# Kernel tuning notes

Measured on AMD Instinct MI355X. Metric: run time of the kernel, lower is better.

Reference implementation:

```python
import jax, jax.numpy as jnp
import numpy as np

BN_EPS = 1e-5


def _bn_relu(x, gamma, beta):
    # training-mode BatchNorm1d over (batch, length) per channel; x: [B,C,N]
    mean = jnp.mean(x, axis=(0, 2), keepdims=True)
    var = jnp.var(x, axis=(0, 2), keepdims=True)  # biased, matching torch normalization
    xh = (x - mean) * jax.lax.rsqrt(var + BN_EPS)
    return jax.nn.relu(xh * gamma[None, :, None] + beta[None, :, None])


def setup_inputs() -> dict:
    key = jax.random.key(0)
    ks = jax.random.split(key, 12)
    B, N, S, C1, C2 = 16, 4096, 1024, 256, 256
    C_in = C1 + C2  # 512
    M0, M1 = 256, 256  # mlp channels
    return {
        "xyz1": jax.random.normal(ks[0], (B, 3, N), dtype=jnp.float32),
        "xyz2": jax.random.normal(ks[1], (B, 3, S), dtype=jnp.float32),
        "points1": jax.random.normal(ks[2], (B, C1, N), dtype=jnp.float32),
        "points2": jax.random.normal(ks[3], (B, C2, S), dtype=jnp.float32),
        "w0": jax.random.normal(ks[4], (M0, C_in), dtype=jnp.float32) * 0.02,
        "b0": jnp.zeros((M0,), dtype=jnp.float32),
        "g0": jnp.ones((M0,), dtype=jnp.float32),
        "be0": jnp.zeros((M0,), dtype=jnp.float32),
        "w1": jax.random.normal(ks[5], (M1, M0), dtype=jnp.float32) * 0.02,
        "b1": jnp.zeros((M1,), dtype=jnp.float32),
        "g1": jnp.ones((M1,), dtype=jnp.float32),
        "be1": jnp.zeros((M1,), dtype=jnp.float32),
    }


def reference(xyz1, xyz2, points1, points2, w0, b0, g0, be0, w1, b1, g1, be1):
    # xyz1: [B,3,N], xyz2: [B,3,S], points1: [B,C1,N], points2: [B,C2,S]
    xyz1_t = xyz1.transpose(0, 2, 1)  # [B,N,3]
    xyz2_t = xyz2.transpose(0, 2, 1)  # [B,S,3]
    p2_t = points2.transpose(0, 2, 1)  # [B,S,C2]

    # squared pairwise distances [B,N,S] via |a|^2 + |b|^2 - 2ab
    d = (jnp.sum(xyz1_t ** 2, -1)[:, :, None]
         + jnp.sum(xyz2_t ** 2, -1)[:, None, :]
         - 2.0 * jnp.einsum('bnd,bsd->bns', xyz1_t, xyz2_t))

    # 3 nearest neighbours (smallest distances)
    neg_d3, idx = jax.lax.top_k(-d, 3)  # [B,N,3]
    dists = -neg_d3

    recip = 1.0 / (dists + 1e-8)
    weight = recip / jnp.sum(recip, axis=-1, keepdims=True)  # [B,N,3]

    gathered = jax.vmap(lambda p, i: p[i])(p2_t, idx)  # [B,N,3,C2]
    interp = jnp.sum(gathered * weight[..., None], axis=2)  # [B,N,C2]

    new_points = jnp.concatenate([points1.transpose(0, 2, 1), interp], axis=-1)  # [B,N,C1+C2]
    x = new_points.transpose(0, 2, 1)  # [B,C_in,N]

    # 1x1 Conv1d == per-position matmul
    x = _bn_relu(jnp.einsum('oi,bin->bon', w0, x) + b0[None, :, None], g0, be0)
    x = _bn_relu(jnp.einsum('oi,bin->bon', w1, x) + b1[None, :, None], g1, be1)
    return x
```

## Files before the change

### kernel.cpp

```cpp
#include <hip/hip_runtime.h>
#include <stdint.h>

using u16 = unsigned short;
using short8 = __attribute__((ext_vector_type(8))) short;
using f32x4  = __attribute__((ext_vector_type(4))) float;
using u32x4  = __attribute__((ext_vector_type(4))) unsigned int;

__device__ __forceinline__ float bf2f(u16 u) {
  return __builtin_bit_cast(float, ((unsigned)u) << 16);
}
__device__ __forceinline__ u16 f2bf(float f) {
  unsigned u = __builtin_bit_cast(unsigned, f);
  u += 0x7FFFu + ((u >> 16) & 1u);
  return (u16)(u >> 16);
}

__device__ __forceinline__ void ins3(float& d0, float& d1, float& d2,
                                     int& i0, int& i1, int& i2, float d, int s) {
  bool c0 = d < d0, c1 = d < d1, c2 = d < d2;
  d2 = c1 ? d1 : (c2 ? d : d2);
  i2 = c1 ? i1 : (c2 ? s : i2);
  d1 = c0 ? d0 : (c1 ? d : d1);
  i1 = c0 ? i0 : (c1 ? s : i1);
  d0 = c0 ? d : d0;
  i0 = c0 ? s : i0;
}

__global__ __launch_bounds__(256, 8) void nn3_kernel(
    const float* __restrict__ xyz1, const float* __restrict__ xyz2,
    int* __restrict__ idx_out, float* __restrict__ w_out) {
  __shared__ __align__(16) float cand[8 * 516];
  const int b = blockIdx.y;
  const int t = threadIdx.x;
  const float* x2 = xyz2 + b * 3072;
  for (int i = t; i < 1024; i += 256) {
    float x = x2[i], y = x2[1024 + i], z = x2[2048 + i];
    f32x4 v = { -2.0f * x, -2.0f * y, -2.0f * z, x*x + y*y + z*z };
    *(f32x4*)&cand[(i >> 7) * 516 + (i & 127) * 4] = v;
  }
  __syncthreads();
  const int q = t >> 3, sub = t & 7;
  const int n = blockIdx.x * 32 + q;
  const float* x1 = xyz1 + b * 12288;
  const float px = x1[n], py = x1[4096 + n], pz = x1[8192 + n];
  float d0 = 1e30f, d1 = 1e30f, d2 = 1e30f;
  int i0 = 0, i1 = 0, i2 = 0;
  const int sbeg = sub << 7;
  const float* reg = &cand[sub * 516];
  #pragma unroll 4
  for (int ii = 0; ii < 128; ++ii) {
    f32x4 c = *(const f32x4*)(reg + ii * 4);
    float d = __builtin_fmaf(px, c[0],
              __builtin_fmaf(py, c[1],
              __builtin_fmaf(pz, c[2], c[3])));
    ins3(d0, d1, d2, i0, i1, i2, d, sbeg + ii);
  }
  for (int st = 1; st <= 4; st <<= 1) {
    float e0 = __shfl_xor(d0, st), e1 = __shfl_xor(d1, st), e2 = __shfl_xor(d2, st);
    int   j0 = __shfl_xor(i0, st), j1 = __shfl_xor(i1, st), j2 = __shfl_xor(i2, st);
    ins3(d0, d1, d2, i0, i1, i2, e0, j0);
    ins3(d0, d1, d2, i0, i1, i2, e1, j1);
    ins3(d0, d1, d2, i0, i1, i2, e2, j2);
  }
  if (sub == 0) {
    const float r1 = px*px + py*py + pz*pz;
    float w0 = 1.0f/(d0 + r1 + 1e-8f), w1 = 1.0f/(d1 + r1 + 1e-8f), w2 = 1.0f/(d2 + r1 + 1e-8f);
    float inv = 1.0f/(w0 + w1 + w2);
    const int pos = b * 4096 + n;
    idx_out[pos*3+0] = i0; idx_out[pos*3+1] = i1; idx_out[pos*3+2] = i2;
    w_out[pos*3+0] = w0*inv; w_out[pos*3+1] = w1*inv; w_out[pos*3+2] = w2*inv;
  }
}

__global__ __launch_bounds__(256) void transpose_cl(
    const float* __restrict__ in, u16* __restrict__ out, int L, int rstride) {
  __shared__ u16 tile[64][66];
  const int b = blockIdx.z;
  in  += (size_t)b * 256 * L;
  out += (size_t)b * L * rstride;
  const int n0 = blockIdx.x * 64, c0 = blockIdx.y * 64;
  const int t = threadIdx.x, ln = t & 63, grp = t >> 6;
  for (int p = 0; p < 16; ++p) {
    int cc = p*4 + grp;
    tile[cc][ln] = f2bf(in[(size_t)(c0 + cc) * L + n0 + ln]);
  }
  __syncthreads();
  for (int p = 0; p < 16; ++p) {
    int nn = p*4 + grp;
    out[(size_t)(n0 + nn) * rstride + c0 + ln] = tile[ln][nn];
  }
}

__global__ __launch_bounds__(256) void cvt_kernel(const float* __restrict__ in,
                                                  u16* __restrict__ out, int n) {
  int i = blockIdx.x * 256 + threadIdx.x;
  if (i < n) out[i] = f2bf(in[i]);
}

__global__ __launch_bounds__(256) void interp_kernel(
    const u16* __restrict__ p2t, const int* __restrict__ idx,
    const float* __restrict__ wgt, u16* __restrict__ A1) {
  const int t = threadIdx.x;
  const int base = blockIdx.x * 16;
  for (int i = 0; i < 16; ++i) {
    const int pos = base + i;
    const int b = pos >> 12;
    const int j0 = idx[pos*3+0], j1 = idx[pos*3+1], j2 = idx[pos*3+2];
    const float w0 = wgt[pos*3+0], w1 = wgt[pos*3+1], w2 = wgt[pos*3+2];
    const u16* r0 = p2t + ((size_t)(b*1024 + j0)) * 256;
    const u16* r1 = p2t + ((size_t)(b*1024 + j1)) * 256;
    const u16* r2 = p2t + ((size_t)(b*1024 + j2)) * 256;
    float v = w0*bf2f(r0[t]) + w1*bf2f(r1[t]) + w2*bf2f(r2[t]);
    A1[(size_t)pos*512 + 256 + t] = f2bf(v);
  }
}

__global__ __launch_bounds__(256) void gemm_kernel(
    const u16* __restrict__ A, const u16* __restrict__ Bw,
    const float* __restrict__ bias, u16* __restrict__ Y, int K) {
  __shared__ __align__(16) u16 As[128*48];
  __shared__ __align__(16) u16 Bs[128*48];
  const int t = threadIdx.x;
  const int m0 = blockIdx.x * 128, n0 = blockIdx.y * 128;
  const int wave = t >> 6, l = t & 63;
  const int wm = wave & 1, wn = wave >> 1;
  const int lc = l & 15, quad = l >> 4;
  f32x4 acc[4][4] = {};
  const int rowA = t >> 2, kc = (t & 3) * 8;
  for (int k0 = 0; k0 < K; k0 += 32) {
    *(u32x4*)&As[rowA*48 + kc]      = *(const u32x4*)&A[(size_t)(m0 + rowA)*K + k0 + kc];
    *(u32x4*)&As[(rowA+64)*48 + kc] = *(const u32x4*)&A[(size_t)(m0 + rowA + 64)*K + k0 + kc];
    *(u32x4*)&Bs[rowA*48 + kc]      = *(const u32x4*)&Bw[(size_t)(n0 + rowA)*K + k0 + kc];
    *(u32x4*)&Bs[(rowA+64)*48 + kc] = *(const u32x4*)&Bw[(size_t)(n0 + rowA + 64)*K + k0 + kc];
    __syncthreads();
    short8 af[4], bfv[4];
    for (int tm = 0; tm < 4; ++tm)
      af[tm] = *(const short8*)&As[(wm*64 + tm*16 + lc)*48 + quad*8];
    for (int tn = 0; tn < 4; ++tn)
      bfv[tn] = *(const short8*)&Bs[(wn*64 + tn*16 + lc)*48 + quad*8];
    for (int tm = 0; tm < 4; ++tm)
      for (int tn = 0; tn < 4; ++tn)
        acc[tm][tn] = __builtin_amdgcn_mfma_f32_16x16x32_bf16(af[tm], bfv[tn], acc[tm][tn], 0, 0, 0);
    __syncthreads();
  }
  for (int tn = 0; tn < 4; ++tn) {
    const int col = n0 + wn*64 + tn*16 + lc;
    const float bb = bias[col];
    for (int tm = 0; tm < 4; ++tm) {
      const int row = m0 + wm*64 + tm*16 + quad*4;
      for (int r = 0; r < 4; ++r)
        Y[(size_t)(row + r)*256 + col] = f2bf(acc[tm][tn][r] + bb);
    }
  }
}

__global__ __launch_bounds__(256) void colstats_kernel(
    const u16* __restrict__ Y, float* __restrict__ sums, float* __restrict__ sumsq) {
  const int t = threadIdx.x;
  size_t base = (size_t)blockIdx.x * 256 * 256;
  float s = 0.0f, q = 0.0f;
  for (int r = 0; r < 256; ++r) {
    float v = bf2f(Y[base + (size_t)r*256 + t]);
    s += v; q += v*v;
  }
  atomicAdd(&sums[t], s);
  atomicAdd(&sumsq[t], q);
}

__global__ void bnprep_kernel(const float* __restrict__ sums, const float* __restrict__ sumsq,
                              const float* __restrict__ g, const float* __restrict__ be,
                              float* __restrict__ scale, float* __restrict__ shift) {
  const int t = threadIdx.x;
  const float inv_n = 1.0f / 65536.0f;
  float mean = sums[t] * inv_n;
  float var = sumsq[t] * inv_n - mean*mean;
  float a = g[t] * rsqrtf(var + 1e-5f);
  scale[t] = a;
  shift[t] = be[t] - mean * a;
}

__global__ __launch_bounds__(256) void bnrelu_kernel(
    const u16* __restrict__ Y, const float* __restrict__ scale,
    const float* __restrict__ shift, u16* __restrict__ X) {
  const int t = threadIdx.x;
  const float a = scale[t], s = shift[t];
  size_t base = (size_t)blockIdx.x * 16 * 256;
  for (int r = 0; r < 16; ++r) {
    float v = bf2f(Y[base + r*256 + t]) * a + s;
    X[base + r*256 + t] = f2bf(v > 0.0f ? v : 0.0f);
  }
}

__global__ __launch_bounds__(256) void bnrelu_tr_kernel(
    const u16* __restrict__ Y, const float* __restrict__ scale,
    const float* __restrict__ shift, float* __restrict__ out) {
  __shared__ u16 tile[256][66];
  const int t = threadIdx.x;
  const int b = blockIdx.z;
  const int n0 = blockIdx.x * 64;
  const float a = scale[t], s = shift[t];
  for (int nn = 0; nn < 64; ++nn) {
    size_t pos = (size_t)b*4096 + n0 + nn;
    float v = bf2f(Y[pos*256 + t]) * a + s;
    tile[t][nn] = f2bf(v > 0.0f ? v : 0.0f);
  }
  __syncthreads();
  const int ln = t & 63, grp = t >> 6;
  for (int p = 0; p < 64; ++p) {
    int oo = p*4 + grp;
    out[((size_t)b*256 + oo)*4096 + n0 + ln] = bf2f(tile[oo][ln]);
  }
}

extern "C" void kernel_launch(void* const* d_in, const int* in_sizes, int n_in,
                              void* d_out, int out_size, void* d_ws, size_t ws_size,
                              hipStream_t stream) {
  const float* xyz1    = (const float*)d_in[0];
  const float* xyz2    = (const float*)d_in[1];
  const float* points1 = (const float*)d_in[2];
  const float* points2 = (const float*)d_in[3];
  const float* w0      = (const float*)d_in[4];
  const float* b0      = (const float*)d_in[5];
  const float* g0      = (const float*)d_in[6];
  const float* be0     = (const float*)d_in[7];
  const float* w1      = (const float*)d_in[8];
  const float* b1      = (const float*)d_in[9];
  const float* g1      = (const float*)d_in[10];
  const float* be1     = (const float*)d_in[11];
  float* out = (float*)d_out;

  char* ws = (char*)d_ws;
  u16*   A1   = (u16*)ws;
  u16*   X0   = (u16*)ws;
  u16*   Y    = (u16*)(ws + (64ull  << 20));
  u16*   p2t  = (u16*)(ws + (96ull  << 20));
  int*   idxb = (int*)(ws + (104ull << 20));
  float* wgtb = (float*)(ws + (105ull << 20));
  u16*   w0b  = (u16*)(ws + (106ull << 20));
  u16*   w1b  = (u16*)(ws + (106ull << 20) + (256u << 10));
  float* stats= (float*)(ws + (106ull << 20) + (512u << 10));

  float* sums0 = stats, *sumsq0 = stats + 256, *scale0 = stats + 512, *shift0 = stats + 768;
  float* sums1 = stats + 1024, *sumsq1 = stats + 1280, *scale1 = stats + 1536, *shift1 = stats + 1792;

  hipMemsetAsync(stats, 0, 2048 * sizeof(float), stream);
  nn3_kernel<<<dim3(128, 16), 256, 0, stream>>>(xyz1, xyz2, idxb, wgtb);
  transpose_cl<<<dim3(16, 4, 16), 256, 0, stream>>>(points2, p2t, 1024, 256);
  transpose_cl<<<dim3(64, 4, 16), 256, 0, stream>>>(points1, A1, 4096, 512);
  cvt_kernel<<<512, 256, 0, stream>>>(w0, w0b, 131072);
  cvt_kernel<<<256, 256, 0, stream>>>(w1, w1b, 65536);
  interp_kernel<<<4096, 256, 0, stream>>>(p2t, idxb, wgtb, A1);
  gemm_kernel<<<dim3(512, 2), 256, 0, stream>>>(A1, w0b, b0, Y, 512);
  colstats_kernel<<<256, 256, 0, stream>>>(Y, sums0, sumsq0);
  bnprep_kernel<<<1, 256, 0, stream>>>(sums0, sumsq0, g0, be0, scale0, shift0);
  bnrelu_kernel<<<4096, 256, 0, stream>>>(Y, scale0, shift0, X0);
  gemm_kernel<<<dim3(512, 2), 256, 0, stream>>>(X0, w1b, b1, Y, 256);
  colstats_kernel<<<256, 256, 0, stream>>>(Y, sums1, sumsq1);
  bnprep_kernel<<<1, 256, 0, stream>>>(sums1, sumsq1, g1, be1, scale1, shift1);
  bnrelu_tr_kernel<<<dim3(64, 1, 16), 256, 0, stream>>>(Y, scale1, shift1, out);
}
```

Baseline: 324.5 us.

## Fuse BN column stats into GEMM epilogue, use direct-to-LDS loads, vectorize BN-ReLU

The GEMM now loads tiles with global_load_lds straight into unpadded LDS, and its epilogue accumulates per-column sum and sum-of-squares, reduced with shuffles and atomics. This removes both separate colstats passes over Y. The bnrelu kernel now processes four channels per thread with 64-bit loads and stores. The cost is more atomics per GEMM block, possible LDS bank conflicts from dropping the padding, and stats computed from fp32 values rather than the rounded bf16 output.

```diff
diff --git a/kernel.cpp b/kernel.cpp
--- a/kernel.cpp
+++ b/kernel.cpp
@@ -5,6 +5,13 @@
 using short8 = __attribute__((ext_vector_type(8))) short;
 using f32x4  = __attribute__((ext_vector_type(4))) float;
 using u32x4  = __attribute__((ext_vector_type(4))) unsigned int;
+
+typedef const __attribute__((address_space(1))) unsigned int gas_u32;
+typedef __attribute__((address_space(3))) unsigned int las_u32;
+
+__device__ __forceinline__ void gload16(const void* g, void* l) {
+  __builtin_amdgcn_global_load_lds((gas_u32*)g, (las_u32*)l, 16, 0, 0);
+}
 
 __device__ __forceinline__ float bf2f(u16 u) {
   return __builtin_bit_cast(float, ((unsigned)u) << 16);
@@ -117,27 +124,33 @@
 
 __global__ __launch_bounds__(256) void gemm_kernel(
     const u16* __restrict__ A, const u16* __restrict__ Bw,
-    const float* __restrict__ bias, u16* __restrict__ Y, int K) {
-  __shared__ __align__(16) u16 As[128*48];
-  __shared__ __align__(16) u16 Bs[128*48];
+    const float* __restrict__ bias, u16* __restrict__ Y, int K,
+    float* __restrict__ sums, float* __restrict__ sumsq) {
+  __shared__ __align__(16) u16 As[128*32];
+  __shared__ __align__(16) u16 Bs[128*32];
   const int t = threadIdx.x;
   const int m0 = blockIdx.x * 128, n0 = blockIdx.y * 128;
   const int wave = t >> 6, l = t & 63;
   const int wm = wave & 1, wn = wave >> 1;
   const int lc = l & 15, quad = l >> 4;
   f32x4 acc[4][4] = {};
-  const int rowA = t >> 2, kc = (t & 3) * 8;
+  const int rA = wave*32 + (l >> 2);
+  const int ko = (l & 3) * 8;
+  u16* ldsA0 = &As[(wave*2 + 0) * 512];
+  u16* ldsA1 = &As[(wave*2 + 1) * 512];
+  u16* ldsB0 = &Bs[(wave*2 + 0) * 512];
+  u16* ldsB1 = &Bs[(wave*2 + 1) * 512];
   for (int k0 = 0; k0 < K; k0 += 32) {
-    *(u32x4*)&As[rowA*48 + kc]      = *(const u32x4*)&A[(size_t)(m0 + rowA)*K + k0 + kc];
-    *(u32x4*)&As[(rowA+64)*48 + kc] = *(const u32x4*)&A[(size_t)(m0 + rowA + 64)*K + k0 + kc];
-    *(u32x4*)&Bs[rowA*48 + kc]      = *(const u32x4*)&Bw[(size_t)(n0 + rowA)*K + k0 + kc];
-    *(u32x4*)&Bs[(rowA+64)*48 + kc] = *(const u32x4*)&Bw[(size_t)(n0 + rowA + 64)*K + k0 + kc];
+    gload16(&A [(size_t)(m0 + rA     )*K + k0 + ko], ldsA0);
+    gload16(&A [(size_t)(m0 + rA + 16)*K + k0 + ko], ldsA1);
+    gload16(&Bw[(size_t)(n0 + rA     )*K + k0 + ko], ldsB0);
+    gload16(&Bw[(size_t)(n0 + rA + 16)*K + k0 + ko], ldsB1);
     __syncthreads();
     short8 af[4], bfv[4];
     for (int tm = 0; tm < 4; ++tm)
-      af[tm] = *(const short8*)&As[(wm*64 + tm*16 + lc)*48 + quad*8];
+      af[tm] = *(const short8*)&As[(wm*64 + tm*16 + lc)*32 + quad*8];
     for (int tn = 0; tn < 4; ++tn)
-      bfv[tn] = *(const short8*)&Bs[(wn*64 + tn*16 + lc)*48 + quad*8];
+      bfv[tn] = *(const short8*)&Bs[(wn*64 + tn*16 + lc)*32 + quad*8];
     for (int tm = 0; tm < 4; ++tm)
       for (int tn = 0; tn < 4; ++tn)
         acc[tm][tn] = __builtin_amdgcn_mfma_f32_16x16x32_bf16(af[tm], bfv[tn], acc[tm][tn], 0, 0, 0);
@@ -146,25 +159,22 @@
   for (int tn = 0; tn < 4; ++tn) {
     const int col = n0 + wn*64 + tn*16 + lc;
     const float bb = bias[col];
+    float s = 0.0f, q = 0.0f;
     for (int tm = 0; tm < 4; ++tm) {
       const int row = m0 + wm*64 + tm*16 + quad*4;
-      for (int r = 0; r < 4; ++r)
-        Y[(size_t)(row + r)*256 + col] = f2bf(acc[tm][tn][r] + bb);
+      for (int r = 0; r < 4; ++r) {
+        float v = acc[tm][tn][r] + bb;
+        Y[(size_t)(row + r)*256 + col] = f2bf(v);
+        s += v; q += v*v;
+      }
     }
-  }
-}
-
-__global__ __launch_bounds__(256) void colstats_kernel(
-    const u16* __restrict__ Y, float* __restrict__ sums, float* __restrict__ sumsq) {
-  const int t = threadIdx.x;
-  size_t base = (size_t)blockIdx.x * 256 * 256;
-  float s = 0.0f, q = 0.0f;
-  for (int r = 0; r < 256; ++r) {
-    float v = bf2f(Y[base + (size_t)r*256 + t]);
-    s += v; q += v*v;
-  }
-  atomicAdd(&sums[t], s);
-  atomicAdd(&sumsq[t], q);
+    s += __shfl_xor(s, 16); s += __shfl_xor(s, 32);
+    q += __shfl_xor(q, 16); q += __shfl_xor(q, 32);
+    if (quad == 0) {
+      atomicAdd(&sums[col],  s);
+      atomicAdd(&sumsq[col], q);
+    }
+  }
 }
 
 __global__ void bnprep_kernel(const float* __restrict__ sums, const float* __restrict__ sumsq,
@@ -183,11 +193,22 @@
     const u16* __restrict__ Y, const float* __restrict__ scale,
     const float* __restrict__ shift, u16* __restrict__ X) {
   const int t = threadIdx.x;
-  const float a = scale[t], s = shift[t];
-  size_t base = (size_t)blockIdx.x * 16 * 256;
-  for (int r = 0; r < 16; ++r) {
-    float v = bf2f(Y[base + r*256 + t]) * a + s;
-    X[base + r*256 + t] = f2bf(v > 0.0f ? v : 0.0f);
+  const int ln = t & 63, grp = t >> 6;
+  const int c0 = ln * 4;
+  const float a0 = scale[c0], a1 = scale[c0+1], a2 = scale[c0+2], a3 = scale[c0+3];
+  const float s0 = shift[c0], s1 = shift[c0+1], s2 = shift[c0+2], s3 = shift[c0+3];
+  size_t row0 = (size_t)blockIdx.x * 64;
+  for (int it = 0; it < 16; ++it) {
+    size_t off = (row0 + it*4 + grp) * 256 + c0;
+    ushort4 v = *(const ushort4*)&Y[off];
+    float f0 = bf2f(v.x)*a0 + s0, f1 = bf2f(v.y)*a1 + s1;
+    float f2v = bf2f(v.z)*a2 + s2, f3 = bf2f(v.w)*a3 + s3;
+    ushort4 o;
+    o.x = f2bf(f0 > 0.0f ? f0 : 0.0f);
+    o.y = f2bf(f1 > 0.0f ? f1 : 0.0f);
+    o.z = f2bf(f2v > 0.0f ? f2v : 0.0f);
+    o.w = f2bf(f3 > 0.0f ? f3 : 0.0f);
+    *(ushort4*)&X[off] = o;
   }
 }
 
@@ -250,12 +271,10 @@
   cvt_kernel<<<512, 256, 0, stream>>>(w0, w0b, 131072);
   cvt_kernel<<<256, 256, 0, stream>>>(w1, w1b, 65536);
   interp_kernel<<<4096, 256, 0, stream>>>(p2t, idxb, wgtb, A1);
-  gemm_kernel<<<dim3(512, 2), 256, 0, stream>>>(A1, w0b, b0, Y, 512);
-  colstats_kernel<<<256, 256, 0, stream>>>(Y, sums0, sumsq0);
+  gemm_kernel<<<dim3(512, 2), 256, 0, stream>>>(A1, w0b, b0, Y, 512, sums0, sumsq0);
   bnprep_kernel<<<1, 256, 0, stream>>>(sums0, sumsq0, g0, be0, scale0, shift0);
-  bnrelu_kernel<<<4096, 256, 0, stream>>>(Y, scale0, shift0, X0);
-  gemm_kernel<<<dim3(512, 2), 256, 0, stream>>>(X0, w1b, b1, Y, 256);
-  colstats_kernel<<<256, 256, 0, stream>>>(Y, sums1, sumsq1);
+  bnrelu_kernel<<<1024, 256, 0, stream>>>(Y, scale0, shift0, X0);
+  gemm_kernel<<<dim3(512, 2), 256, 0, stream>>>(X0, w1b, b1, Y, 256, sums1, sumsq1);
   bnprep_kernel<<<1, 256, 0, stream>>>(sums1, sumsq1, g1, be1, scale1, shift1);
   bnrelu_tr_kernel<<<dim3(64, 1, 16), 256, 0, stream>>>(Y, scale1, shift1, out);
 }
```

Result: slower. 385.3 us (+18.7%).
